# Kernel tuning notes

Hardware: AMD Instinct MI355X
Metric: run time of the kernel (lower is better)

The kernel has to match this reference:

```python
import jax, jax.numpy as jnp
import numpy as np

NUM_ITERATIONS = 5
EPSILON_0 = 1.0
EPS = 1e-20


def setup_inputs() -> dict:
    key = jax.random.key(0)
    k1, k2 = jax.random.split(key)
    B, NIN, NOUT = 8192, 3072, 512
    x = jax.random.uniform(k1, (B, NIN), dtype=jnp.float32)
    w = jax.random.uniform(k2, (NOUT, NIN), dtype=jnp.float32)
    # weights setter normalizes rows to sum to 1
    w = w / w.sum(axis=1, keepdims=True)
    h_initial = jnp.full((NOUT,), 1.0 / NOUT, dtype=jnp.float32)
    return {"x": x, "weights": w, "h_initial": h_initial}


def reference(x, weights, h_initial):
    # x: [B, NIN], weights: [NOUT, NIN], h_initial: [NOUT]
    x = x / (x.sum(axis=1, keepdims=True) + EPS)  # input normalization in forward()
    B = x.shape[0]
    h = jnp.broadcast_to(h_initial[None, :], (B, h_initial.shape[0]))

    def step(h, _):
        # Original: h_w = h[:,:,None]*W[None]; h_w /= h_w.sum(1,keepdim)+eps;
        #           h_w = (h_w * x[:,None,:]).sum(-1)
        # Equivalent without materializing [B, NOUT, NIN]:
        denom = h @ weights                       # [B, NIN] = sum_n h_bn W_nk
        h_w = h * ((x / (denom + EPS)) @ weights.T)  # [B, NOUT]
        h_new = h + EPSILON_0 * h_w               # epsilon_0 > 0 branch
        h_new = h_new / (h_new.sum(axis=1, keepdims=True) + EPS)
        return h_new, None

    h, _ = jax.lax.scan(step, h, None, length=NUM_ITERATIONS)
    return h
```

## Files before the change

kernel.cpp:

```cpp
#include <hip/hip_runtime.h>


#define NIN 3072
#define NOUT 512

using f32x4 = __attribute__((ext_vector_type(4))) float;
using i32x8 = __attribute__((ext_vector_type(8))) int;

union frag32 { i32x8 v; uint4 q[2]; };

#define MFMA128(A, B, C) \
    __builtin_amdgcn_mfma_scale_f32_16x16x128_f8f6f4( \
        (A), (B), (C), 0, 0, 0, (int)0x7f7f7f7f, 0, (int)0x7f7f7f7f)
#define MFMA128_F6(A, B, C) \
    __builtin_amdgcn_mfma_scale_f32_16x16x128_f8f6f4( \
        (A), (B), (C), 0, 2, 0, (int)0x7f7f7f7f, 0, (int)0x7f7f7f7f)

__device__ __forceinline__ unsigned short f2bf(float f) {
    unsigned int u = __builtin_bit_cast(unsigned int, f);
    return (unsigned short)((u + 0x7fffu + ((u >> 16) & 1u)) >> 16);
}
__device__ __forceinline__ float bf2f(unsigned short s) {
    unsigned int u = ((unsigned int)s) << 16;
    return __builtin_bit_cast(float, u);
}

__device__ __forceinline__ unsigned enc_fp6(float p) {
    if (p < 1.9375f) {
        int q = (int)rintf(p * 8.0f);
        return (unsigned)q;
    }
    if (p < 3.875f) {
        int m = (int)rintf((p - 2.0f) * 4.0f);
        return (m > 7) ? 24u : (16u + (unsigned)m);
    }
    int m = (int)rintf((p - 4.0f) * 2.0f);
    if (m > 7) m = 7;
    return 24u + (unsigned)m;
}

__device__ __forceinline__ void load6(frag32& f, const unsigned char* p) {
    const uint2* q = reinterpret_cast<const uint2*>(p);
    uint2 a = q[0], b = q[1], c = q[2];
    f.v = (i32x8){(int)a.x, (int)a.y, (int)b.x, (int)b.y, (int)c.x, (int)c.y, 0, 0};
}

#define LDS_BARRIER() do {                                   \
    asm volatile("s_waitcnt lgkmcnt(0)" ::: "memory");       \
    __builtin_amdgcn_s_barrier();                            \
    asm volatile("" ::: "memory");                           \
} while (0)

__global__ void prep_all(const float* __restrict__ x,
                         const float* __restrict__ W,
                         const float* __restrict__ h_init,
                         unsigned short* __restrict__ X2,
                         unsigned char* __restrict__ W1,
                         unsigned char* __restrict__ W2,
                         float* __restrict__ d0inv) {
    __shared__ float wsum[4];
    __shared__ float dred[8][32];
    const int bb = blockIdx.x;
    const int t  = threadIdx.x;

    if (bb < 8192) {
        const int b = bb;
        const float4* r4 = reinterpret_cast<const float4*>(x + (size_t)b * NIN);
        float s = 0.f;
        float4 v0 = r4[t], v1 = r4[t + 256], v2 = r4[t + 512];
        s = v0.x + v0.y + v0.z + v0.w + v1.x + v1.y + v1.z + v1.w + v2.x + v2.y + v2.z + v2.w;
        #pragma unroll
        for (int off = 32; off > 0; off >>= 1) s += __shfl_down(s, off, 64);
        int w = t >> 6, l = t & 63;
        if (l == 0) wsum[w] = s;
        __syncthreads();
        float inv = 16.0f / (wsum[0] + wsum[1] + wsum[2] + wsum[3] + 1e-20f);
        unsigned short* orow = X2 + (size_t)b * NIN;
        #pragma unroll
        for (int c = 0; c < 3; ++c) {
            float4 v = (c == 0) ? v0 : (c == 1) ? v1 : v2;
            ushort4 o;
            o.x = f2bf(v.x * inv); o.y = f2bf(v.y * inv);
            o.z = f2bf(v.z * inv); o.w = f2bf(v.w * inv);
            *reinterpret_cast<ushort4*>(orow + (t + c * 256) * 4) = o;
        }
    } else if (bb < 8192 + 384) {
        int tt = (bb - 8192) * 256 + t;
        if (tt < 49152) {
            int l = tt & 63, g = tt >> 6;
            int s = g >> 5, rem = g & 31, w = rem >> 2, nt = rem & 3;
            int n = w * 64 + nt * 16 + (l & 15);
            int kbase = s * 128 + ((l >> 4) << 5);
            const float* src = W + (size_t)n * NIN + kbase;
            unsigned int words[8];
            #pragma unroll
            for (int q = 0; q < 8; ++q) {
                float v0 = src[q * 4 + 0] * 4096.0f, v1 = src[q * 4 + 1] * 4096.0f;
                float v2 = src[q * 4 + 2] * 4096.0f, v3 = src[q * 4 + 3] * 4096.0f;
                int pk = __builtin_amdgcn_cvt_pk_fp8_f32(v0, v1, 0, false);
                pk     = __builtin_amdgcn_cvt_pk_fp8_f32(v2, v3, pk, true);
                words[q] = (unsigned int)pk;
            }
            uint4* dst = reinterpret_cast<uint4*>(W2 + (size_t)tt * 32);
            dst[0] = *reinterpret_cast<uint4*>(&words[0]);
            dst[1] = *reinterpret_cast<uint4*>(&words[4]);
        } else {
            int u = tt - 49152;
            int l = u & 63, g = u >> 6;
            int c = g & 3, sw = g >> 2;
            int w = sw & 7, s = sw >> 3;
            int kout = s * 128 + w * 16 + (l & 15);
            int nbase = c * 128 + ((l >> 4) << 5);
            float v[32];
            #pragma unroll
            for (int j = 0; j < 32; ++j)
                v[j] = W[(size_t)(nbase + j) * NIN + kout] * 8192.0f;
            unsigned int dw[6] = {0, 0, 0, 0, 0, 0};
            #pragma unroll
            for (int j = 0; j < 32; ++j) {
                unsigned c6 = enc_fp6(v[j]);
                int bit = 6 * j, di = bit >> 5, off = bit & 31;
                dw[di] |= c6 << off;
                if (off > 26) dw[di + 1] |= c6 >> (32 - off);
            }
            uint2* d2 = reinterpret_cast<uint2*>(W1 + (size_t)u * 24);
            d2[0] = make_uint2(dw[0], dw[1]);
            d2[1] = make_uint2(dw[2], dw[3]);
            d2[2] = make_uint2(dw[4], dw[5]);
        }
    } else {
        int kb = bb - 8576;
        int kid = t & 31, nsub = t >> 5;
        int k = kb * 32 + kid;
        int n0 = nsub * 64;
        float s = 0.f;
        const float* p = W + (size_t)n0 * NIN + k;
        #pragma unroll 8
        for (int n = 0; n < 64; ++n) s += h_init[n0 + n] * p[(size_t)n * NIN];
        dred[nsub][kid] = s;
        __syncthreads();
        if (t < 32) {
            float sm = 1e-20f;
            #pragma unroll
            for (int j = 0; j < 8; ++j) sm += dred[j][t];
            d0inv[kb * 32 + t] = 1.0f / sm;
        }
    }
}

__global__ __launch_bounds__(512, 1) void nnmf_main(
    const unsigned short* __restrict__ X2,
    const unsigned char* __restrict__ W1,
    const unsigned char* __restrict__ W2,
    const float* __restrict__ d0inv,
    const float* __restrict__ h_init,
    float* __restrict__ out)
{
    __shared__ unsigned char  h8_lds[32 * 528];
    __shared__ float          h32_lds[32 * 516];
    __shared__ unsigned short x_lds[32 * 136];
    __shared__ unsigned char  r8_lds[32 * 144];
    __shared__ float red[8][32];

    const int tid = threadIdx.x;
    const int w  = tid >> 6;
    const int l  = tid & 63;
    const int lo = l & 15;
    const int hi = l >> 4;
    const int b0 = blockIdx.x * 32;

    for (int idx = tid; idx < 32 * 512; idx += 512) {
        int r = idx >> 9, c = idx & 511;
        h32_lds[r * 516 + c] = h_init[c];
    }

    const int xrow = tid >> 4, xcc = tid & 15;
    const uint4* xg = reinterpret_cast<const uint4*>(X2 + (size_t)(b0 + xrow) * NIN + xcc * 8);
    unsigned short* xdst = &x_lds[xrow * 136 + xcc * 8];

    const unsigned char* w1base = W1 + ((size_t)(w * 4) * 64 + l) * 24;
    const unsigned char* w2base = W2 + (size_t)w * 8192 + (size_t)l * 32;

    *reinterpret_cast<uint4*>(xdst) = xg[0];
    uint4 xnext = xg[16];
    frag32 w1buf[4];
    __syncthreads();

    const float DSCL = 4.76837158203125e-07f;
    const float TS   = 1.0f / 65536.0f;
    f32x4 tacc[2][4];

    for (int it = 0; it < 5; ++it) {
        #pragma unroll
        for (int m = 0; m < 2; ++m)
            #pragma unroll
            for (int nt = 0; nt < 4; ++nt)
                tacc[m][nt] = (f32x4){0.f, 0.f, 0.f, 0.f};

        for (int s = 0; s < 24; ++s) {
            const int sn  = (s + 1 == 24) ? 0 : s + 1;
            const int sn2 = (s + 2 >= 24) ? (s + 2 - 24) : s + 2;

            frag32 w2v[4];
            {
                const unsigned char* w2p = w2base + (size_t)s * 65536;
                #pragma unroll
                for (int nt = 0; nt < 4; ++nt) {
                    const uint4* p = reinterpret_cast<const uint4*>(w2p + nt * 2048);
                    w2v[nt].q[0] = p[0];
                    w2v[nt].q[1] = p[1];
                }
            }

            f32x4 d0 = {0,0,0,0}, d1 = {0,0,0,0};
            float dv = 0.f;
            if (it == 0) {
                dv = d0inv[s * 128 + w * 16 + lo];
            } else {
                #pragma unroll
                for (int c = 0; c < 4; ++c) {
                    frag32 ha0, ha1;
                    const uint4* p0 = reinterpret_cast<const uint4*>(
                        &h8_lds[lo * 528 + c * 128 + hi * 32]);
                    const uint4* p1 = reinterpret_cast<const uint4*>(
                        &h8_lds[(16 + lo) * 528 + c * 128 + hi * 32]);
                    ha0.q[0] = p0[0]; ha0.q[1] = p0[1];
                    ha1.q[0] = p1[0]; ha1.q[1] = p1[1];
                    d0 = MFMA128_F6(ha0.v, w1buf[c].v, d0);
                    d1 = MFMA128_F6(ha1.v, w1buf[c].v, d1);
                }
            }

            #pragma unroll
            for (int i = 0; i < 4; ++i) {
                int row0 = hi * 4 + i;
                float x0 = bf2f(x_lds[row0 * 136 + w * 16 + lo]);
                float x1 = bf2f(x_lds[(16 + row0) * 136 + w * 16 + lo]);
                float r0, r1;
                if (it == 0) { r0 = x0 * dv; r1 = x1 * dv; }
                else {
                    r0 = x0 * __builtin_amdgcn_rcpf(fmaf(d0[i], DSCL, 1e-20f));
                    r1 = x1 * __builtin_amdgcn_rcpf(fmaf(d1[i], DSCL, 1e-20f));
                }
                int c0 = __builtin_amdgcn_cvt_pk_fp8_f32(r0, r0, 0, false);
                int c1 = __builtin_amdgcn_cvt_pk_fp8_f32(r1, r1, 0, false);
                r8_lds[row0 * 144 + w * 16 + lo] = (unsigned char)(c0 & 0xff);
                r8_lds[(16 + row0) * 144 + w * 16 + lo] = (unsigned char)(c1 & 0xff);
            }
            LDS_BARRIER();

            frag32 ra0, ra1;
            {
                const uint4* p0 = reinterpret_cast<const uint4*>(&r8_lds[lo * 144 + hi * 32]);
                const uint4* p1 = reinterpret_cast<const uint4*>(&r8_lds[(16 + lo) * 144 + hi * 32]);
                ra0.q[0] = p0[0]; ra0.q[1] = p0[1];
                ra1.q[0] = p1[0]; ra1.q[1] = p1[1];
            }
            #pragma unroll
            for (int nt = 0; nt < 2; ++nt) {
                tacc[0][nt] = MFMA128(ra0.v, w2v[nt].v, tacc[0][nt]);
                tacc[1][nt] = MFMA128(ra1.v, w2v[nt].v, tacc[1][nt]);
            }

            if (it > 0 || s == 23) {
                const unsigned char* w1p = w1base + (size_t)sn * 49152;
                #pragma unroll
                for (int c = 0; c < 4; ++c)
                    load6(w1buf[c], w1p + c * 1536);
            }

            #pragma unroll
            for (int nt = 2; nt < 4; ++nt) {
                tacc[0][nt] = MFMA128(ra0.v, w2v[nt].v, tacc[0][nt]);
                tacc[1][nt] = MFMA128(ra1.v, w2v[nt].v, tacc[1][nt]);
            }

            *reinterpret_cast<uint4*>(xdst) = xnext;
            xnext = xg[(size_t)sn2 * 16];
            LDS_BARRIER();
        }

        float hv_[2][4][4];
        float p[2][4];
        #pragma unroll
        for (int m = 0; m < 2; ++m)
            #pragma unroll
            for (int i = 0; i < 4; ++i) p[m][i] = 0.f;

        #pragma unroll
        for (int m = 0; m < 2; ++m)
            #pragma unroll
            for (int nt = 0; nt < 4; ++nt)
                #pragma unroll
                for (int i = 0; i < 4; ++i) {
                    int row = m * 16 + hi * 4 + i;
                    int col = w * 64 + nt * 16 + lo;
                    float hv = h32_lds[row * 516 + col];
                    float v = hv * (1.f + tacc[m][nt][i] * TS);
                    hv_[m][nt][i] = v;
                    p[m][i] += v;
                }
        #pragma unroll
        for (int mask = 1; mask < 16; mask <<= 1)
            #pragma unroll
            for (int m = 0; m < 2; ++m)
                #pragma unroll
                for (int i = 0; i < 4; ++i)
                    p[m][i] += __shfl_xor(p[m][i], mask, 64);
        if (lo == 0) {
            #pragma unroll
            for (int m = 0; m < 2; ++m)
                #pragma unroll
                for (int i = 0; i < 4; ++i)
                    red[w][m * 16 + hi * 4 + i] = p[m][i];
        }
        __syncthreads();
        float inv[2][4];
        #pragma unroll
        for (int m = 0; m < 2; ++m)
            #pragma unroll
            for (int i = 0; i < 4; ++i) {
                int row = m * 16 + hi * 4 + i;
                float S = 0.f;
                #pragma unroll
                for (int ww = 0; ww < 8; ++ww) S += red[ww][row];
                inv[m][i] = 1.f / (S + 1e-20f);
            }

        if (it < 4) {
            #pragma unroll
            for (int m = 0; m < 2; ++m)
                #pragma unroll
                for (int nt = 0; nt < 4; ++nt)
                    #pragma unroll
                    for (int i = 0; i < 4; ++i) {
                        int row = m * 16 + hi * 4 + i;
                        int col = w * 64 + nt * 16 + lo;
                        float hv = hv_[m][nt][i] * inv[m][i];
                        h32_lds[row * 516 + col] = hv;
                        int c = __builtin_amdgcn_cvt_pk_fp8_f32(hv * 256.0f, hv * 256.0f, 0, false);
                        h8_lds[row * 528 + col] = (unsigned char)(c & 0xff);
                    }
            __syncthreads();
        } else {
            #pragma unroll
            for (int m = 0; m < 2; ++m)
                #pragma unroll
                for (int nt = 0; nt < 4; ++nt)
                    #pragma unroll
                    for (int i = 0; i < 4; ++i) {
                        int row = m * 16 + hi * 4 + i;
                        int col = w * 64 + nt * 16 + lo;
                        out[(size_t)(b0 + row) * 512 + col] = hv_[m][nt][i] * inv[m][i];
                    }
        }
    }
}

extern "C" void kernel_launch(void* const* d_in, const int* in_sizes, int n_in,
                              void* d_out, int out_size, void* d_ws, size_t ws_size,
                              hipStream_t stream) {
    const float* x   = (const float*)d_in[0];
    const float* wgt = (const float*)d_in[1];
    const float* h0  = (const float*)d_in[2];
    float* out = (float*)d_out;

    unsigned short* X2 = (unsigned short*)d_ws;
    unsigned char*  W1 = (unsigned char*)((char*)d_ws + 50331648);
    unsigned char*  W2 = (unsigned char*)((char*)d_ws + 51511296);
    float* d0inv       = (float*)((char*)d_ws + 53084160);

    prep_all<<<8672, 256, 0, stream>>>(x, wgt, h0, X2, W1, W2, d0inv);
    nnmf_main<<<256, 512, 0, stream>>>(X2, W1, W2, d0inv, h0, out);
}
```

Before: 381.3 us.

## Split main kernel work across 16 waves and keep h in registers

Doubles the block to 1024 threads (16 waves). Each wave now handles one 16-row half of the batch tile for the denominator MFMA and two 16-column output tiles for the numerator GEMM, and the W2 fp8 packing layout is changed to match the new per-wave column order. The fp32 h state moves from an LDS array into per-thread registers, which removes the h32 LDS traffic and frees shared memory. The intent is more latency hiding with less work per wave, at the cost of more barrier participants, a wider 16-way row reduction and lower register budget per thread.

```diff
diff --git a/kernel.cpp b/kernel.cpp
--- a/kernel.cpp
+++ b/kernel.cpp
@@ -88,8 +88,8 @@
         int tt = (bb - 8192) * 256 + t;
         if (tt < 49152) {
             int l = tt & 63, g = tt >> 6;
-            int s = g >> 5, rem = g & 31, w = rem >> 2, nt = rem & 3;
-            int n = w * 64 + nt * 16 + (l & 15);
+            int s = g >> 5, ntile = g & 31;
+            int n = ntile * 16 + (l & 15);
             int kbase = s * 128 + ((l >> 4) << 5);
             const float* src = W + (size_t)n * NIN + kbase;
             unsigned int words[8];
@@ -148,7 +148,7 @@
     }
 }
 
-__global__ __launch_bounds__(512, 1) void nnmf_main(
+__global__ __launch_bounds__(1024, 1) void nnmf_main(
     const unsigned short* __restrict__ X2,
     const unsigned char* __restrict__ W1,
     const unsigned char* __restrict__ W2,
@@ -157,95 +157,92 @@
     float* __restrict__ out)
 {
     __shared__ unsigned char  h8_lds[32 * 528];
-    __shared__ float          h32_lds[32 * 516];
     __shared__ unsigned short x_lds[32 * 136];
     __shared__ unsigned char  r8_lds[32 * 144];
-    __shared__ float red[8][32];
+    __shared__ float red[16][32];
 
     const int tid = threadIdx.x;
-    const int w  = tid >> 6;
-    const int l  = tid & 63;
-    const int lo = l & 15;
-    const int hi = l >> 4;
+    const int w     = tid >> 6;
+    const int l     = tid & 63;
+    const int lo    = l & 15;
+    const int hi    = l >> 4;
+    const int w8    = w & 7;
+    const int mhalf = w >> 3;
     const int b0 = blockIdx.x * 32;
 
-    for (int idx = tid; idx < 32 * 512; idx += 512) {
-        int r = idx >> 9, c = idx & 511;
-        h32_lds[r * 516 + c] = h_init[c];
-    }
-
-    const int xrow = tid >> 4, xcc = tid & 15;
-    const uint4* xg = reinterpret_cast<const uint4*>(X2 + (size_t)(b0 + xrow) * NIN + xcc * 8);
-    unsigned short* xdst = &x_lds[xrow * 136 + xcc * 8];
-
-    const unsigned char* w1base = W1 + ((size_t)(w * 4) * 64 + l) * 24;
-    const unsigned char* w2base = W2 + (size_t)w * 8192 + (size_t)l * 32;
-
-    *reinterpret_cast<uint4*>(xdst) = xg[0];
-    uint4 xnext = xg[16];
+    float h_reg[2][2][4];
+    #pragma unroll
+    for (int j = 0; j < 2; ++j) {
+        float hv = h_init[(2 * w + j) * 16 + lo];
+        #pragma unroll
+        for (int m = 0; m < 2; ++m)
+            #pragma unroll
+            for (int i = 0; i < 4; ++i)
+                h_reg[m][j][i] = hv;
+    }
+
+    const int xrow = tid >> 5, xcc = tid & 31;
+    const uint2* xg = reinterpret_cast<const uint2*>(X2 + (size_t)(b0 + xrow) * NIN) + xcc;
+    unsigned short* xdst = &x_lds[xrow * 136 + xcc * 4];
+
+    const unsigned char* w1base = W1 + ((size_t)(w8 * 4) * 64 + l) * 24;
+    const unsigned char* w2base = W2 + ((size_t)(2 * w) * 64 + l) * 32;
+
+    *reinterpret_cast<uint2*>(xdst) = xg[0];
+    uint2 xnext = xg[32];
     frag32 w1buf[4];
     __syncthreads();
 
     const float DSCL = 4.76837158203125e-07f;
     const float TS   = 1.0f / 65536.0f;
-    f32x4 tacc[2][4];
+    f32x4 tacc[2][2];
 
     for (int it = 0; it < 5; ++it) {
         #pragma unroll
         for (int m = 0; m < 2; ++m)
             #pragma unroll
-            for (int nt = 0; nt < 4; ++nt)
-                tacc[m][nt] = (f32x4){0.f, 0.f, 0.f, 0.f};
+            for (int j = 0; j < 2; ++j)
+                tacc[m][j] = (f32x4){0.f, 0.f, 0.f, 0.f};
 
         for (int s = 0; s < 24; ++s) {
             const int sn  = (s + 1 == 24) ? 0 : s + 1;
             const int sn2 = (s + 2 >= 24) ? (s + 2 - 24) : s + 2;
 
-            frag32 w2v[4];
+            frag32 w2v[2];
             {
                 const unsigned char* w2p = w2base + (size_t)s * 65536;
                 #pragma unroll
-                for (int nt = 0; nt < 4; ++nt) {
-                    const uint4* p = reinterpret_cast<const uint4*>(w2p + nt * 2048);
-                    w2v[nt].q[0] = p[0];
-                    w2v[nt].q[1] = p[1];
+                for (int j = 0; j < 2; ++j) {
+                    const uint4* p = reinterpret_cast<const uint4*>(w2p + j * 2048);
+                    w2v[j].q[0] = p[0];
+                    w2v[j].q[1] = p[1];
                 }
             }
 
-            f32x4 d0 = {0,0,0,0}, d1 = {0,0,0,0};
+            f32x4 d = {0,0,0,0};
             float dv = 0.f;
             if (it == 0) {
-                dv = d0inv[s * 128 + w * 16 + lo];
+                dv = d0inv[s * 128 + w8 * 16 + lo];
             } else {
                 #pragma unroll
                 for (int c = 0; c < 4; ++c) {
-                    frag32 ha0, ha1;
-                    const uint4* p0 = reinterpret_cast<const uint4*>(
-                        &h8_lds[lo * 528 + c * 128 + hi * 32]);
-                    const uint4* p1 = reinterpret_cast<const uint4*>(
-                        &h8_lds[(16 + lo) * 528 + c * 128 + hi * 32]);
-                    ha0.q[0] = p0[0]; ha0.q[1] = p0[1];
-                    ha1.q[0] = p1[0]; ha1.q[1] = p1[1];
-                    d0 = MFMA128_F6(ha0.v, w1buf[c].v, d0);
-                    d1 = MFMA128_F6(ha1.v, w1buf[c].v, d1);
+                    frag32 ha;
+                    const uint4* p = reinterpret_cast<const uint4*>(
+                        &h8_lds[(mhalf * 16 + lo) * 528 + c * 128 + hi * 32]);
+                    ha.q[0] = p[0]; ha.q[1] = p[1];
+                    d = MFMA128_F6(ha.v, w1buf[c].v, d);
                 }
             }
 
             #pragma unroll
             for (int i = 0; i < 4; ++i) {
-                int row0 = hi * 4 + i;
-                float x0 = bf2f(x_lds[row0 * 136 + w * 16 + lo]);
-                float x1 = bf2f(x_lds[(16 + row0) * 136 + w * 16 + lo]);
-                float r0, r1;
-                if (it == 0) { r0 = x0 * dv; r1 = x1 * dv; }
-                else {
-                    r0 = x0 * __builtin_amdgcn_rcpf(fmaf(d0[i], DSCL, 1e-20f));
-                    r1 = x1 * __builtin_amdgcn_rcpf(fmaf(d1[i], DSCL, 1e-20f));
-                }
-                int c0 = __builtin_amdgcn_cvt_pk_fp8_f32(r0, r0, 0, false);
-                int c1 = __builtin_amdgcn_cvt_pk_fp8_f32(r1, r1, 0, false);
-                r8_lds[row0 * 144 + w * 16 + lo] = (unsigned char)(c0 & 0xff);
-                r8_lds[(16 + row0) * 144 + w * 16 + lo] = (unsigned char)(c1 & 0xff);
+                int row = mhalf * 16 + hi * 4 + i;
+                float xv = bf2f(x_lds[row * 136 + w8 * 16 + lo]);
+                float r;
+                if (it == 0) r = xv * dv;
+                else         r = xv * __builtin_amdgcn_rcpf(fmaf(d[i], DSCL, 1e-20f));
+                int c0 = __builtin_amdgcn_cvt_pk_fp8_f32(r, r, 0, false);
+                r8_lds[row * 144 + w8 * 16 + lo] = (unsigned char)(c0 & 0xff);
             }
             LDS_BARRIER();
 
@@ -256,11 +253,8 @@
                 ra0.q[0] = p0[0]; ra0.q[1] = p0[1];
                 ra1.q[0] = p1[0]; ra1.q[1] = p1[1];
             }
-            #pragma unroll
-            for (int nt = 0; nt < 2; ++nt) {
-                tacc[0][nt] = MFMA128(ra0.v, w2v[nt].v, tacc[0][nt]);
-                tacc[1][nt] = MFMA128(ra1.v, w2v[nt].v, tacc[1][nt]);
-            }
+            tacc[0][0] = MFMA128(ra0.v, w2v[0].v, tacc[0][0]);
+            tacc[1][0] = MFMA128(ra1.v, w2v[0].v, tacc[1][0]);
 
             if (it > 0 || s == 23) {
                 const unsigned char* w1p = w1base + (size_t)sn * 49152;
@@ -269,18 +263,15 @@
                     load6(w1buf[c], w1p + c * 1536);
             }
 
-            #pragma unroll
-            for (int nt = 2; nt < 4; ++nt) {
-                tacc[0][nt] = MFMA128(ra0.v, w2v[nt].v, tacc[0][nt]);
-                tacc[1][nt] = MFMA128(ra1.v, w2v[nt].v, tacc[1][nt]);
-            }
-
-            *reinterpret_cast<uint4*>(xdst) = xnext;
-            xnext = xg[(size_t)sn2 * 16];
+            tacc[0][1] = MFMA128(ra0.v, w2v[1].v, tacc[0][1]);
+            tacc[1][1] = MFMA128(ra1.v, w2v[1].v, tacc[1][1]);
+
+            *reinterpret_cast<uint2*>(xdst) = xnext;
+            xnext = xg[(size_t)sn2 * 32];
             LDS_BARRIER();
         }
 
-        float hv_[2][4][4];
+        float hv_[2][2][4];
         float p[2][4];
         #pragma unroll
         for (int m = 0; m < 2; ++m)
@@ -290,14 +281,11 @@
         #pragma unroll
         for (int m = 0; m < 2; ++m)
             #pragma unroll
-            for (int nt = 0; nt < 4; ++nt)
+            for (int j = 0; j < 2; ++j)
                 #pragma unroll
                 for (int i = 0; i < 4; ++i) {
-                    int row = m * 16 + hi * 4 + i;
-                    int col = w * 64 + nt * 16 + lo;
-                    float hv = h32_lds[row * 516 + col];
-                    float v = hv * (1.f + tacc[m][nt][i] * TS);
-                    hv_[m][nt][i] = v;
+                    float v = h_reg[m][j][i] * (1.f + tacc[m][j][i] * TS);
+                    hv_[m][j][i] = v;
                     p[m][i] += v;
                 }
         #pragma unroll
@@ -323,7 +311,7 @@
                 int row = m * 16 + hi * 4 + i;
                 float S = 0.f;
                 #pragma unroll
-                for (int ww = 0; ww < 8; ++ww) S += red[ww][row];
+                for (int ww = 0; ww < 16; ++ww) S += red[ww][row];
                 inv[m][i] = 1.f / (S + 1e-20f);
             }
 
@@ -331,13 +319,13 @@
             #pragma unroll
             for (int m = 0; m < 2; ++m)
                 #pragma unroll
-                for (int nt = 0; nt < 4; ++nt)
+                for (int j = 0; j < 2; ++j)
                     #pragma unroll
                     for (int i = 0; i < 4; ++i) {
                         int row = m * 16 + hi * 4 + i;
-                        int col = w * 64 + nt * 16 + lo;
-                        float hv = hv_[m][nt][i] * inv[m][i];
-                        h32_lds[row * 516 + col] = hv;
+                        int col = (2 * w + j) * 16 + lo;
+                        float hv = hv_[m][j][i] * inv[m][i];
+                        h_reg[m][j][i] = hv;
                         int c = __builtin_amdgcn_cvt_pk_fp8_f32(hv * 256.0f, hv * 256.0f, 0, false);
                         h8_lds[row * 528 + col] = (unsigned char)(c & 0xff);
                     }
@@ -346,12 +334,12 @@
             #pragma unroll
             for (int m = 0; m < 2; ++m)
                 #pragma unroll
-                for (int nt = 0; nt < 4; ++nt)
+                for (int j = 0; j < 2; ++j)
                     #pragma unroll
                     for (int i = 0; i < 4; ++i) {
                         int row = m * 16 + hi * 4 + i;
-                        int col = w * 64 + nt * 16 + lo;
-                        out[(size_t)(b0 + row) * 512 + col] = hv_[m][nt][i] * inv[m][i];
+                        int col = (2 * w + j) * 16 + lo;
+                        out[(size_t)(b0 + row) * 512 + col] = hv_[m][j][i] * inv[m][i];
                     }
         }
     }
@@ -371,5 +359,5 @@
     float* d0inv       = (float*)((char*)d_ws + 53084160);
 
     prep_all<<<8672, 256, 0, stream>>>(x, wgt, h0, X2, W1, W2, d0inv);
-    nnmf_main<<<256, 512, 0, stream>>>(X2, W1, W2, d0inv, h0, out);
-}
+    nnmf_main<<<256, 1024, 0, stream>>>(X2, W1, W2, d0inv, h0, out);
+}
```

After: 590.0 us. 1.55x slower.

## Stage weight tiles in LDS to build FP8/FP6 packs and initial denominators together

Applied to the files above, without the earlier changes.

The prep kernel now loads each 64x128 weight tile once into shared memory with coalesced float4 reads. From that tile it builds the FP8 W2 fragments, the transposed FP6 W1 fragments and partial h_init·W sums, replacing three separate passes that used strided, uncoalesced global reads. The final reduction of the 8 partial denominators and the reciprocal move into the main kernel's first iteration. The change also adds a 64x132 float LDS tile to every prep block, including the x-normalization blocks, which may lower their occupancy.

```diff
diff --git a/kernel.cpp b/kernel.cpp
--- a/kernel.cpp
+++ b/kernel.cpp
@@ -57,14 +57,81 @@
                          unsigned short* __restrict__ X2,
                          unsigned char* __restrict__ W1,
                          unsigned char* __restrict__ W2,
-                         float* __restrict__ d0inv) {
+                         float* __restrict__ d0part) {
+    __shared__ float tile[64][132];
     __shared__ float wsum[4];
-    __shared__ float dred[8][32];
     const int bb = blockIdx.x;
     const int t  = threadIdx.x;
 
-    if (bb < 8192) {
-        const int b = bb;
+    if (bb < 192) {
+        const int s  = bb >> 3, nc = bb & 7;
+        const int n0 = nc * 64, k0 = s * 128;
+
+        {
+            int r8 = t >> 5, c4 = (t & 31) << 2;
+            #pragma unroll
+            for (int pass = 0; pass < 8; ++pass) {
+                int r = pass * 8 + r8;
+                float4 v = *reinterpret_cast<const float4*>(
+                    &W[(size_t)(n0 + r) * NIN + k0 + c4]);
+                tile[r][c4] = v.x; tile[r][c4 + 1] = v.y;
+                tile[r][c4 + 2] = v.z; tile[r][c4 + 3] = v.w;
+            }
+        }
+        __syncthreads();
+
+        {
+            int ntl = t >> 6, l = t & 63, lo = l & 15, hi = l >> 4;
+            int n_loc = ntl * 16 + lo;
+            int kk = hi * 32;
+            unsigned int words[8];
+            #pragma unroll
+            for (int q = 0; q < 8; ++q) {
+                float v0 = tile[n_loc][kk + q * 4 + 0] * 4096.0f;
+                float v1 = tile[n_loc][kk + q * 4 + 1] * 4096.0f;
+                float v2 = tile[n_loc][kk + q * 4 + 2] * 4096.0f;
+                float v3 = tile[n_loc][kk + q * 4 + 3] * 4096.0f;
+                int pk = __builtin_amdgcn_cvt_pk_fp8_f32(v0, v1, 0, false);
+                pk     = __builtin_amdgcn_cvt_pk_fp8_f32(v2, v3, pk, true);
+                words[q] = (unsigned int)pk;
+            }
+            uint4* dst = reinterpret_cast<uint4*>(
+                W2 + ((size_t)((s * 32 + nc * 4 + ntl) * 64 + l)) * 32);
+            dst[0] = *reinterpret_cast<uint4*>(&words[0]);
+            dst[1] = *reinterpret_cast<uint4*>(&words[4]);
+        }
+
+        {
+            int w8 = t >> 5, r5 = t & 31, l15 = r5 & 15, hs = r5 >> 4;
+            int hi = ((nc & 1) << 1) + hs;
+            int l  = hi * 16 + l15;
+            int c  = nc >> 1;
+            int kout_loc = w8 * 16 + l15;
+            unsigned int dw[6] = {0, 0, 0, 0, 0, 0};
+            #pragma unroll
+            for (int j = 0; j < 32; ++j) {
+                float p = tile[hs * 32 + j][kout_loc] * 8192.0f;
+                unsigned c6 = enc_fp6(p);
+                int bit = 6 * j, di = bit >> 5, off = bit & 31;
+                dw[di] |= c6 << off;
+                if (off > 26) dw[di + 1] |= c6 >> (32 - off);
+            }
+            uint2* d2 = reinterpret_cast<uint2*>(
+                W1 + ((size_t)(((s * 8 + w8) * 4 + c) * 64 + l)) * 24);
+            d2[0] = make_uint2(dw[0], dw[1]);
+            d2[1] = make_uint2(dw[2], dw[3]);
+            d2[2] = make_uint2(dw[4], dw[5]);
+        }
+
+        if (t < 128) {
+            float ssum = 0.f;
+            #pragma unroll 8
+            for (int r = 0; r < 64; ++r)
+                ssum += h_init[n0 + r] * tile[r][t];
+            d0part[(size_t)nc * NIN + k0 + t] = ssum;
+        }
+    } else {
+        const int b = bb - 192;
         const float4* r4 = reinterpret_cast<const float4*>(x + (size_t)b * NIN);
         float s = 0.f;
         float4 v0 = r4[t], v1 = r4[t + 256], v2 = r4[t + 512];
@@ -84,67 +151,6 @@
             o.z = f2bf(v.z * inv); o.w = f2bf(v.w * inv);
             *reinterpret_cast<ushort4*>(orow + (t + c * 256) * 4) = o;
         }
-    } else if (bb < 8192 + 384) {
-        int tt = (bb - 8192) * 256 + t;
-        if (tt < 49152) {
-            int l = tt & 63, g = tt >> 6;
-            int s = g >> 5, rem = g & 31, w = rem >> 2, nt = rem & 3;
-            int n = w * 64 + nt * 16 + (l & 15);
-            int kbase = s * 128 + ((l >> 4) << 5);
-            const float* src = W + (size_t)n * NIN + kbase;
-            unsigned int words[8];
-            #pragma unroll
-            for (int q = 0; q < 8; ++q) {
-                float v0 = src[q * 4 + 0] * 4096.0f, v1 = src[q * 4 + 1] * 4096.0f;
-                float v2 = src[q * 4 + 2] * 4096.0f, v3 = src[q * 4 + 3] * 4096.0f;
-                int pk = __builtin_amdgcn_cvt_pk_fp8_f32(v0, v1, 0, false);
-                pk     = __builtin_amdgcn_cvt_pk_fp8_f32(v2, v3, pk, true);
-                words[q] = (unsigned int)pk;
-            }
-            uint4* dst = reinterpret_cast<uint4*>(W2 + (size_t)tt * 32);
-            dst[0] = *reinterpret_cast<uint4*>(&words[0]);
-            dst[1] = *reinterpret_cast<uint4*>(&words[4]);
-        } else {
-            int u = tt - 49152;
-            int l = u & 63, g = u >> 6;
-            int c = g & 3, sw = g >> 2;
-            int w = sw & 7, s = sw >> 3;
-            int kout = s * 128 + w * 16 + (l & 15);
-            int nbase = c * 128 + ((l >> 4) << 5);
-            float v[32];
-            #pragma unroll
-            for (int j = 0; j < 32; ++j)
-                v[j] = W[(size_t)(nbase + j) * NIN + kout] * 8192.0f;
-            unsigned int dw[6] = {0, 0, 0, 0, 0, 0};
-            #pragma unroll
-            for (int j = 0; j < 32; ++j) {
-                unsigned c6 = enc_fp6(v[j]);
-                int bit = 6 * j, di = bit >> 5, off = bit & 31;
-                dw[di] |= c6 << off;
-                if (off > 26) dw[di + 1] |= c6 >> (32 - off);
-            }
-            uint2* d2 = reinterpret_cast<uint2*>(W1 + (size_t)u * 24);
-            d2[0] = make_uint2(dw[0], dw[1]);
-            d2[1] = make_uint2(dw[2], dw[3]);
-            d2[2] = make_uint2(dw[4], dw[5]);
-        }
-    } else {
-        int kb = bb - 8576;
-        int kid = t & 31, nsub = t >> 5;
-        int k = kb * 32 + kid;
-        int n0 = nsub * 64;
-        float s = 0.f;
-        const float* p = W + (size_t)n0 * NIN + k;
-        #pragma unroll 8
-        for (int n = 0; n < 64; ++n) s += h_init[n0 + n] * p[(size_t)n * NIN];
-        dred[nsub][kid] = s;
-        __syncthreads();
-        if (t < 32) {
-            float sm = 1e-20f;
-            #pragma unroll
-            for (int j = 0; j < 8; ++j) sm += dred[j][t];
-            d0inv[kb * 32 + t] = 1.0f / sm;
-        }
     }
 }
 
@@ -152,7 +158,7 @@
     const unsigned short* __restrict__ X2,
     const unsigned char* __restrict__ W1,
     const unsigned char* __restrict__ W2,
-    const float* __restrict__ d0inv,
+    const float* __restrict__ d0part,
     const float* __restrict__ h_init,
     float* __restrict__ out)
 {
@@ -215,7 +221,11 @@
             f32x4 d0 = {0,0,0,0}, d1 = {0,0,0,0};
             float dv = 0.f;
             if (it == 0) {
-                dv = d0inv[s * 128 + w * 16 + lo];
+                const float* dp = d0part + s * 128 + w * 16 + lo;
+                float sm = 1e-20f;
+                #pragma unroll
+                for (int j = 0; j < 8; ++j) sm += dp[(size_t)j * NIN];
+                dv = 1.0f / sm;
             } else {
                 #pragma unroll
                 for (int c = 0; c < 4; ++c) {
@@ -368,8 +378,8 @@
     unsigned short* X2 = (unsigned short*)d_ws;
     unsigned char*  W1 = (unsigned char*)((char*)d_ws + 50331648);
     unsigned char*  W2 = (unsigned char*)((char*)d_ws + 51511296);
-    float* d0inv       = (float*)((char*)d_ws + 53084160);
-
-    prep_all<<<8672, 256, 0, stream>>>(x, wgt, h0, X2, W1, W2, d0inv);
-    nnmf_main<<<256, 512, 0, stream>>>(X2, W1, W2, d0inv, h0, out);
-}
+    float* d0part      = (float*)((char*)d_ws + 53084160);
+
+    prep_all<<<8384, 256, 0, stream>>>(x, wgt, h0, X2, W1, W2, d0part);
+    nnmf_main<<<256, 512, 0, stream>>>(X2, W1, W2, d0part, h0, out);
+}
```

Result: no change. 388.0 us (+1.8%).

## Halve batch tile to 16 rows per block and launch 512 blocks

Applied to the files above, without the earlier changes.

Each block now handles 16 batch rows instead of 32. The grid doubles to 512 blocks, and launch bounds allow 2 blocks per CU. This fills all CUs (256 blocks left CUs idle on a 256-CU part) and adds occupancy to hide latency. In exchange, each weight fragment loaded from global/L2 feeds half as many MFMAs, so total weight traffic doubles. The h8_lds array still holds 32 rows, which is wasted LDS.

```diff
diff --git a/kernel.cpp b/kernel.cpp
--- a/kernel.cpp
+++ b/kernel.cpp
@@ -148,7 +148,7 @@
     }
 }
 
-__global__ __launch_bounds__(512, 1) void nnmf_main(
+__global__ __launch_bounds__(512, 2) void nnmf_main(
     const unsigned short* __restrict__ X2,
     const unsigned char* __restrict__ W1,
     const unsigned char* __restrict__ W2,
@@ -157,45 +157,43 @@
     float* __restrict__ out)
 {
     __shared__ unsigned char  h8_lds[32 * 528];
-    __shared__ float          h32_lds[32 * 516];
-    __shared__ unsigned short x_lds[32 * 136];
-    __shared__ unsigned char  r8_lds[32 * 144];
-    __shared__ float red[8][32];
+    __shared__ float          h32_lds[16 * 516];
+    __shared__ unsigned short x_lds[16 * 136];
+    __shared__ unsigned char  r8_lds[16 * 144];
+    __shared__ float red[8][16];
 
     const int tid = threadIdx.x;
     const int w  = tid >> 6;
     const int l  = tid & 63;
     const int lo = l & 15;
     const int hi = l >> 4;
-    const int b0 = blockIdx.x * 32;
-
-    for (int idx = tid; idx < 32 * 512; idx += 512) {
+    const int b0 = blockIdx.x * 16;
+
+    for (int idx = tid; idx < 16 * 512; idx += 512) {
         int r = idx >> 9, c = idx & 511;
         h32_lds[r * 516 + c] = h_init[c];
     }
 
-    const int xrow = tid >> 4, xcc = tid & 15;
-    const uint4* xg = reinterpret_cast<const uint4*>(X2 + (size_t)(b0 + xrow) * NIN + xcc * 8);
-    unsigned short* xdst = &x_lds[xrow * 136 + xcc * 8];
+    const int xrow = tid >> 5, xcc = tid & 31;
+    const uint2* xg = reinterpret_cast<const uint2*>(X2 + (size_t)(b0 + xrow) * NIN) + xcc;
+    unsigned short* xdst = &x_lds[xrow * 136 + xcc * 4];
 
     const unsigned char* w1base = W1 + ((size_t)(w * 4) * 64 + l) * 24;
     const unsigned char* w2base = W2 + (size_t)w * 8192 + (size_t)l * 32;
 
-    *reinterpret_cast<uint4*>(xdst) = xg[0];
-    uint4 xnext = xg[16];
+    *reinterpret_cast<uint2*>(xdst) = xg[0];
+    uint2 xnext = xg[32];
     frag32 w1buf[4];
     __syncthreads();
 
     const float DSCL = 4.76837158203125e-07f;
     const float TS   = 1.0f / 65536.0f;
-    f32x4 tacc[2][4];
+    f32x4 tacc[4];
 
     for (int it = 0; it < 5; ++it) {
         #pragma unroll
-        for (int m = 0; m < 2; ++m)
-            #pragma unroll
-            for (int nt = 0; nt < 4; ++nt)
-                tacc[m][nt] = (f32x4){0.f, 0.f, 0.f, 0.f};
+        for (int nt = 0; nt < 4; ++nt)
+            tacc[nt] = (f32x4){0.f, 0.f, 0.f, 0.f};
 
         for (int s = 0; s < 24; ++s) {
             const int sn  = (s + 1 == 24) ? 0 : s + 1;
@@ -212,22 +210,18 @@
                 }
             }
 
-            f32x4 d0 = {0,0,0,0}, d1 = {0,0,0,0};
+            f32x4 d0 = {0,0,0,0};
             float dv = 0.f;
             if (it == 0) {
                 dv = d0inv[s * 128 + w * 16 + lo];
             } else {
                 #pragma unroll
                 for (int c = 0; c < 4; ++c) {
-                    frag32 ha0, ha1;
-                    const uint4* p0 = reinterpret_cast<const uint4*>(
+                    frag32 ha;
+                    const uint4* p = reinterpret_cast<const uint4*>(
                         &h8_lds[lo * 528 + c * 128 + hi * 32]);
-                    const uint4* p1 = reinterpret_cast<const uint4*>(
-                        &h8_lds[(16 + lo) * 528 + c * 128 + hi * 32]);
-                    ha0.q[0] = p0[0]; ha0.q[1] = p0[1];
-                    ha1.q[0] = p1[0]; ha1.q[1] = p1[1];
-                    d0 = MFMA128_F6(ha0.v, w1buf[c].v, d0);
-                    d1 = MFMA128_F6(ha1.v, w1buf[c].v, d1);
+                    ha.q[0] = p[0]; ha.q[1] = p[1];
+                    d0 = MFMA128_F6(ha.v, w1buf[c].v, d0);
                 }
             }
 
@@ -235,32 +229,22 @@
             for (int i = 0; i < 4; ++i) {
                 int row0 = hi * 4 + i;
                 float x0 = bf2f(x_lds[row0 * 136 + w * 16 + lo]);
-                float x1 = bf2f(x_lds[(16 + row0) * 136 + w * 16 + lo]);
-                float r0, r1;
-                if (it == 0) { r0 = x0 * dv; r1 = x1 * dv; }
-                else {
-                    r0 = x0 * __builtin_amdgcn_rcpf(fmaf(d0[i], DSCL, 1e-20f));
-                    r1 = x1 * __builtin_amdgcn_rcpf(fmaf(d1[i], DSCL, 1e-20f));
-                }
+                float r0;
+                if (it == 0) r0 = x0 * dv;
+                else         r0 = x0 * __builtin_amdgcn_rcpf(fmaf(d0[i], DSCL, 1e-20f));
                 int c0 = __builtin_amdgcn_cvt_pk_fp8_f32(r0, r0, 0, false);
-                int c1 = __builtin_amdgcn_cvt_pk_fp8_f32(r1, r1, 0, false);
                 r8_lds[row0 * 144 + w * 16 + lo] = (unsigned char)(c0 & 0xff);
-                r8_lds[(16 + row0) * 144 + w * 16 + lo] = (unsigned char)(c1 & 0xff);
             }
             LDS_BARRIER();
 
-            frag32 ra0, ra1;
+            frag32 ra0;
             {
                 const uint4* p0 = reinterpret_cast<const uint4*>(&r8_lds[lo * 144 + hi * 32]);
-                const uint4* p1 = reinterpret_cast<const uint4*>(&r8_lds[(16 + lo) * 144 + hi * 32]);
                 ra0.q[0] = p0[0]; ra0.q[1] = p0[1];
-                ra1.q[0] = p1[0]; ra1.q[1] = p1[1];
-            }
-            #pragma unroll
-            for (int nt = 0; nt < 2; ++nt) {
-                tacc[0][nt] = MFMA128(ra0.v, w2v[nt].v, tacc[0][nt]);
-                tacc[1][nt] = MFMA128(ra1.v, w2v[nt].v, tacc[1][nt]);
-            }
+            }
+            #pragma unroll
+            for (int nt = 0; nt < 2; ++nt)
+                tacc[nt] = MFMA128(ra0.v, w2v[nt].v, tacc[nt]);
 
             if (it > 0 || s == 23) {
                 const unsigned char* w1p = w1base + (size_t)sn * 49152;
@@ -270,89 +254,73 @@
             }
 
             #pragma unroll
-            for (int nt = 2; nt < 4; ++nt) {
-                tacc[0][nt] = MFMA128(ra0.v, w2v[nt].v, tacc[0][nt]);
-                tacc[1][nt] = MFMA128(ra1.v, w2v[nt].v, tacc[1][nt]);
-            }
-
-            *reinterpret_cast<uint4*>(xdst) = xnext;
-            xnext = xg[(size_t)sn2 * 16];
+            for (int nt = 2; nt < 4; ++nt)
+                tacc[nt] = MFMA128(ra0.v, w2v[nt].v, tacc[nt]);
+
+            *reinterpret_cast<uint2*>(xdst) = xnext;
+            xnext = xg[(size_t)sn2 * 32];
             LDS_BARRIER();
         }
 
-        float hv_[2][4][4];
-        float p[2][4];
-        #pragma unroll
-        for (int m = 0; m < 2; ++m)
-            #pragma unroll
-            for (int i = 0; i < 4; ++i) p[m][i] = 0.f;
-
-        #pragma unroll
-        for (int m = 0; m < 2; ++m)
+        float hv_[4][4];
+        float p[4];
+        #pragma unroll
+        for (int i = 0; i < 4; ++i) p[i] = 0.f;
+
+        #pragma unroll
+        for (int nt = 0; nt < 4; ++nt)
+            #pragma unroll
+            for (int i = 0; i < 4; ++i) {
+                int row = hi * 4 + i;
+                int col = w * 64 + nt * 16 + lo;
+                float hv = h32_lds[row * 516 + col];
+                float v = hv * (1.f + tacc[nt][i] * TS);
+                hv_[nt][i] = v;
+                p[i] += v;
+            }
+        #pragma unroll
+        for (int mask = 1; mask < 16; mask <<= 1)
+            #pragma unroll
+            for (int i = 0; i < 4; ++i)
+                p[i] += __shfl_xor(p[i], mask, 64);
+        if (lo == 0) {
+            #pragma unroll
+            for (int i = 0; i < 4; ++i)
+                red[w][hi * 4 + i] = p[i];
+        }
+        __syncthreads();
+        float inv[4];
+        #pragma unroll
+        for (int i = 0; i < 4; ++i) {
+            int row = hi * 4 + i;
+            float S = 0.f;
+            #pragma unroll
+            for (int ww = 0; ww < 8; ++ww) S += red[ww][row];
+            inv[i] = 1.f / (S + 1e-20f);
+        }
+
+        if (it < 4) {
             #pragma unroll
             for (int nt = 0; nt < 4; ++nt)
                 #pragma unroll
                 for (int i = 0; i < 4; ++i) {
-                    int row = m * 16 + hi * 4 + i;
+                    int row = hi * 4 + i;
                     int col = w * 64 + nt * 16 + lo;
-                    float hv = h32_lds[row * 516 + col];
-                    float v = hv * (1.f + tacc[m][nt][i] * TS);
-                    hv_[m][nt][i] = v;
-                    p[m][i] += v;
+                    float hv = hv_[nt][i] * inv[i];
+                    h32_lds[row * 516 + col] = hv;
+                    int c = __builtin_amdgcn_cvt_pk_fp8_f32(hv * 256.0f, hv * 256.0f, 0, false);
+                    h8_lds[row * 528 + col] = (unsigned char)(c & 0xff);
                 }
-        #pragma unroll
-        for (int mask = 1; mask < 16; mask <<= 1)
-            #pragma unroll
-            for (int m = 0; m < 2; ++m)
-                #pragma unroll
-                for (int i = 0; i < 4; ++i)
-                    p[m][i] += __shfl_xor(p[m][i], mask, 64);
-        if (lo == 0) {
-            #pragma unroll
-            for (int m = 0; m < 2; ++m)
-                #pragma unroll
-                for (int i = 0; i < 4; ++i)
-                    red[w][m * 16 + hi * 4 + i] = p[m][i];
-        }
-        __syncthreads();
-        float inv[2][4];
-        #pragma unroll
-        for (int m = 0; m < 2; ++m)
-            #pragma unroll
-            for (int i = 0; i < 4; ++i) {
-                int row = m * 16 + hi * 4 + i;
-                float S = 0.f;
-                #pragma unroll
-                for (int ww = 0; ww < 8; ++ww) S += red[ww][row];
-                inv[m][i] = 1.f / (S + 1e-20f);
-            }
-
-        if (it < 4) {
-            #pragma unroll
-            for (int m = 0; m < 2; ++m)
-                #pragma unroll
-                for (int nt = 0; nt < 4; ++nt)
-                    #pragma unroll
-                    for (int i = 0; i < 4; ++i) {
-                        int row = m * 16 + hi * 4 + i;
-                        int col = w * 64 + nt * 16 + lo;
-                        float hv = hv_[m][nt][i] * inv[m][i];
-                        h32_lds[row * 516 + col] = hv;
-                        int c = __builtin_amdgcn_cvt_pk_fp8_f32(hv * 256.0f, hv * 256.0f, 0, false);
-                        h8_lds[row * 528 + col] = (unsigned char)(c & 0xff);
-                    }
             __syncthreads();
         } else {
             #pragma unroll
-            for (int m = 0; m < 2; ++m)
-                #pragma unroll
-                for (int nt = 0; nt < 4; ++nt)
-                    #pragma unroll
-                    for (int i = 0; i < 4; ++i) {
-                        int row = m * 16 + hi * 4 + i;
-                        int col = w * 64 + nt * 16 + lo;
-                        out[(size_t)(b0 + row) * 512 + col] = hv_[m][nt][i] * inv[m][i];
-                    }
+            for (int nt = 0; nt < 4; ++nt)
+                #pragma unroll
+                for (int i = 0; i < 4; ++i) {
+                    int row = hi * 4 + i;
+                    int col = w * 64 + nt * 16 + lo;
+                    out[(size_t)(b0 + row) * 512 + col] = hv_[nt][i] * inv[i];
+                }
         }
     }
 }
@@ -371,5 +339,5 @@
     float* d0inv       = (float*)((char*)d_ws + 53084160);
 
     prep_all<<<8672, 256, 0, stream>>>(x, wgt, h0, X2, W1, W2, d0inv);
-    nnmf_main<<<256, 512, 0, stream>>>(X2, W1, W2, d0inv, h0, out);
-}
+    nnmf_main<<<512, 512, 0, stream>>>(X2, W1, W2, d0inv, h0, out);
+}
```

Result: slower. 530.1 us (+39.0%).
